# Kernel tuning notes

Hardware: AMD Instinct MI355X
Metric: run time of the kernel (lower is better)

Reference implementation:

```python
import jax, jax.numpy as jnp
import numpy as np

INPUT_SIZE = 4
HIDDEN = 2048
OUTPUT_SIZE = 2
NOISE_STD = 0.05
ALPHA = 0.2
RANK = 2
N_SUPPORTS = 2
GDIM = 2 * RANK + INPUT_SIZE  # gaussian_basis_dim default
BATCH = 32
SEQ = 1000


def setup_inputs() -> dict:
    key = jax.random.key(0)
    ks = jax.random.split(key, 8)
    inp = jax.random.normal(ks[0], (BATCH, SEQ, INPUT_SIZE), dtype=jnp.float32)
    noise = jax.random.normal(ks[1], (BATCH, SEQ, HIDDEN), dtype=jnp.float32)
    gaussian_basis = jax.random.normal(ks[2], (GDIM, HIDDEN), dtype=jnp.float32)
    # supports: block indicator masks over hidden units (equal split, weights=None)
    sup = np.zeros((N_SUPPORTS, HIDDEN), dtype=np.float32)
    l = HIDDEN // N_SUPPORTS
    for i in range(N_SUPPORTS):
        sup[i, l * i:l * (i + 1)] = 1.0
    supports = jnp.asarray(sup)
    wi_weights = jax.random.normal(ks[3], (INPUT_SIZE, N_SUPPORTS, GDIM), dtype=jnp.float32)
    m_weights = jax.random.normal(ks[4], (RANK, N_SUPPORTS, GDIM), dtype=jnp.float32) / jnp.sqrt(jnp.float32(HIDDEN))
    n_weights = jax.random.normal(ks[5], (RANK, N_SUPPORTS, GDIM), dtype=jnp.float32) / jnp.sqrt(jnp.float32(HIDDEN))
    wo_weights = jax.random.normal(ks[6], (OUTPUT_SIZE, N_SUPPORTS, GDIM), dtype=jnp.float32) / jnp.float32(HIDDEN)
    wi_biases = jnp.zeros((INPUT_SIZE, N_SUPPORTS), dtype=jnp.float32)
    m_biases = jnp.zeros((RANK, N_SUPPORTS), dtype=jnp.float32)
    n_biases = jnp.zeros((RANK, N_SUPPORTS), dtype=jnp.float32)
    h0_weights = jnp.zeros((N_SUPPORTS, GDIM), dtype=jnp.float32)
    return {
        "input": inp, "noise": noise,
        "wi_weights": wi_weights, "m_weights": m_weights, "n_weights": n_weights,
        "wo_weights": wo_weights, "wi_biases": wi_biases, "m_biases": m_biases,
        "n_biases": n_biases, "h0_weights": h0_weights,
        "gaussian_basis": gaussian_basis, "supports": supports,
    }


def _proxy_params(wi_weights, m_weights, n_weights, wo_weights,
                  wi_biases, m_biases, n_biases, h0_weights,
                  gaussian_basis, supports):
    # (X, S, G) @ (G, H) -> (X, S, H); mask by supports (S, H); sum over S
    def mix(w):
        return jnp.einsum('xsg,gh->xsh', w, gaussian_basis)
    wi = jnp.sum(mix(wi_weights) * supports, axis=1) + wi_biases @ supports      # (I, H)
    m = (jnp.sum(mix(m_weights) * supports, axis=1) + m_biases @ supports).T     # (H, R)
    n = (jnp.sum(mix(n_weights) * supports, axis=1) + n_biases @ supports).T     # (H, R)
    wo = jnp.sum(mix(wo_weights) * supports, axis=1).T                            # (H, O)
    h0 = jnp.sum((h0_weights @ gaussian_basis) * supports, axis=0)                # (H,)
    return wi, m, n, wo, h0


def reference(input, noise, wi_weights, m_weights, n_weights, wo_weights,
              wi_biases, m_biases, n_biases, h0_weights, gaussian_basis, supports):
    wi, m, n, wo, h0 = _proxy_params(wi_weights, m_weights, n_weights, wo_weights,
                                     wi_biases, m_biases, n_biases, h0_weights,
                                     gaussian_basis, supports)
    B = input.shape[0]
    # Precompute external input projection for all steps: (B, T, H)
    xin = jnp.einsum('bti,ih->bth', input, wi)
    h_init = jnp.broadcast_to(h0, (B, h0.shape[0]))
    r_init = jnp.tanh(h_init)

    noise_T = jnp.swapaxes(noise, 0, 1)  # (T, B, H)
    xin_T = jnp.swapaxes(xin, 0, 1)      # (T, B, H)

    def step(carry, xs):
        h, r = carry
        noise_t, xin_t = xs
        h = h + NOISE_STD * noise_t + ALPHA * (-h + (r @ n) @ m.T + xin_t)
        r = jnp.tanh(h)
        return (h, r), r

    _, rs = jax.lax.scan(step, (h_init, r_init), (noise_T, xin_T))  # rs: (T, B, H)
    output = jnp.einsum('tbh,ho->bto', rs, wo)  # (B, T, O)
    return output
```

## Files before the change

kernel.cpp:

```cpp
#include <hip/hip_runtime.h>

#define BATCH 32
#define SEQT 1000
#define INSZ 4
#define HID 2048
#define NOISE_STD 0.05f
#define ALPHA 0.2f
#define ONE_M_ALPHA (1.0f - ALPHA)

#define NTHREADS 256
#define NWAVES 4
#define EPT 8
#define NPAIR 4
#define PF 4

typedef float v2f __attribute__((ext_vector_type(2)));

__device__ __forceinline__ v2f pk_fma(v2f a, v2f b, v2f c) {
    v2f d; asm("v_pk_fma_f32 %0, %1, %2, %3" : "=v"(d) : "v"(a), "v"(b), "v"(c)); return d;
}
__device__ __forceinline__ v2f pk_mul(v2f a, v2f b) {
    v2f d; asm("v_pk_mul_f32 %0, %1, %2" : "=v"(d) : "v"(a), "v"(b)); return d;
}
__device__ __forceinline__ v2f pk_add(v2f a, v2f b) {
    v2f d; asm("v_pk_add_f32 %0, %1, %2" : "=v"(d) : "v"(a), "v"(b)); return d;
}
#define C2(v) (v2f{(v), (v)})

__device__ __forceinline__ void tree64_quad(float& a, float& b, float& c, float& d) {
    asm("s_nop 1\n\t"
        "v_add_f32_dpp %0, %0, %0 row_shr:1 row_mask:0xf bank_mask:0xf bound_ctrl:0\n\t"
        "v_add_f32_dpp %1, %1, %1 row_shr:1 row_mask:0xf bank_mask:0xf bound_ctrl:0\n\t"
        "v_add_f32_dpp %2, %2, %2 row_shr:1 row_mask:0xf bank_mask:0xf bound_ctrl:0\n\t"
        "v_add_f32_dpp %3, %3, %3 row_shr:1 row_mask:0xf bank_mask:0xf bound_ctrl:0\n\t"
        "v_add_f32_dpp %0, %0, %0 row_shr:2 row_mask:0xf bank_mask:0xf bound_ctrl:0\n\t"
        "v_add_f32_dpp %1, %1, %1 row_shr:2 row_mask:0xf bank_mask:0xf bound_ctrl:0\n\t"
        "v_add_f32_dpp %2, %2, %2 row_shr:2 row_mask:0xf bank_mask:0xf bound_ctrl:0\n\t"
        "v_add_f32_dpp %3, %3, %3 row_shr:2 row_mask:0xf bank_mask:0xf bound_ctrl:0\n\t"
        "v_add_f32_dpp %0, %0, %0 row_shr:4 row_mask:0xf bank_mask:0xf bound_ctrl:0\n\t"
        "v_add_f32_dpp %1, %1, %1 row_shr:4 row_mask:0xf bank_mask:0xf bound_ctrl:0\n\t"
        "v_add_f32_dpp %2, %2, %2 row_shr:4 row_mask:0xf bank_mask:0xf bound_ctrl:0\n\t"
        "v_add_f32_dpp %3, %3, %3 row_shr:4 row_mask:0xf bank_mask:0xf bound_ctrl:0\n\t"
        "v_add_f32_dpp %0, %0, %0 row_shr:8 row_mask:0xf bank_mask:0xf bound_ctrl:0\n\t"
        "v_add_f32_dpp %1, %1, %1 row_shr:8 row_mask:0xf bank_mask:0xf bound_ctrl:0\n\t"
        "v_add_f32_dpp %2, %2, %2 row_shr:8 row_mask:0xf bank_mask:0xf bound_ctrl:0\n\t"
        "v_add_f32_dpp %3, %3, %3 row_shr:8 row_mask:0xf bank_mask:0xf bound_ctrl:0\n\t"
        "v_add_f32_dpp %0, %0, %0 row_bcast:15 row_mask:0xf bank_mask:0xf bound_ctrl:0\n\t"
        "v_add_f32_dpp %1, %1, %1 row_bcast:15 row_mask:0xf bank_mask:0xf bound_ctrl:0\n\t"
        "v_add_f32_dpp %2, %2, %2 row_bcast:15 row_mask:0xf bank_mask:0xf bound_ctrl:0\n\t"
        "v_add_f32_dpp %3, %3, %3 row_bcast:15 row_mask:0xf bank_mask:0xf bound_ctrl:0\n\t"
        "v_add_f32_dpp %0, %0, %0 row_bcast:31 row_mask:0xf bank_mask:0xf bound_ctrl:0\n\t"
        "v_add_f32_dpp %1, %1, %1 row_bcast:31 row_mask:0xf bank_mask:0xf bound_ctrl:0\n\t"
        "v_add_f32_dpp %2, %2, %2 row_bcast:31 row_mask:0xf bank_mask:0xf bound_ctrl:0\n\t"
        "v_add_f32_dpp %3, %3, %3 row_bcast:31 row_mask:0xf bank_mask:0xf bound_ctrl:0"
        : "+v"(a), "+v"(b), "+v"(c), "+v"(d));
}

__device__ __forceinline__ void tree64_pair(float& a, float& b) {
    asm("s_nop 1\n\t"
        "v_add_f32_dpp %0, %0, %0 row_shr:1 row_mask:0xf bank_mask:0xf bound_ctrl:0\n\t"
        "v_add_f32_dpp %1, %1, %1 row_shr:1 row_mask:0xf bank_mask:0xf bound_ctrl:0\n\t"
        "v_add_f32_dpp %0, %0, %0 row_shr:2 row_mask:0xf bank_mask:0xf bound_ctrl:0\n\t"
        "v_add_f32_dpp %1, %1, %1 row_shr:2 row_mask:0xf bank_mask:0xf bound_ctrl:0\n\t"
        "v_add_f32_dpp %0, %0, %0 row_shr:4 row_mask:0xf bank_mask:0xf bound_ctrl:0\n\t"
        "v_add_f32_dpp %1, %1, %1 row_shr:4 row_mask:0xf bank_mask:0xf bound_ctrl:0\n\t"
        "v_add_f32_dpp %0, %0, %0 row_shr:8 row_mask:0xf bank_mask:0xf bound_ctrl:0\n\t"
        "v_add_f32_dpp %1, %1, %1 row_shr:8 row_mask:0xf bank_mask:0xf bound_ctrl:0\n\t"
        "v_add_f32_dpp %0, %0, %0 row_bcast:15 row_mask:0xf bank_mask:0xf bound_ctrl:0\n\t"
        "v_add_f32_dpp %1, %1, %1 row_bcast:15 row_mask:0xf bank_mask:0xf bound_ctrl:0\n\t"
        "v_add_f32_dpp %0, %0, %0 row_bcast:31 row_mask:0xf bank_mask:0xf bound_ctrl:0\n\t"
        "v_add_f32_dpp %1, %1, %1 row_bcast:31 row_mask:0xf bank_mask:0xf bound_ctrl:0"
        : "+v"(a), "+v"(b));
}

__device__ __forceinline__ void bfly4_quad(float& a, float& b, float& c, float& d) {
    asm("s_nop 1\n\t"
        "v_add_f32_dpp %0, %0, %0 quad_perm:[1,0,3,2] row_mask:0xf bank_mask:0xf\n\t"
        "v_add_f32_dpp %1, %1, %1 quad_perm:[1,0,3,2] row_mask:0xf bank_mask:0xf\n\t"
        "v_add_f32_dpp %2, %2, %2 quad_perm:[1,0,3,2] row_mask:0xf bank_mask:0xf\n\t"
        "v_add_f32_dpp %3, %3, %3 quad_perm:[1,0,3,2] row_mask:0xf bank_mask:0xf\n\t"
        "v_add_f32_dpp %0, %0, %0 quad_perm:[2,3,0,1] row_mask:0xf bank_mask:0xf\n\t"
        "v_add_f32_dpp %1, %1, %1 quad_perm:[2,3,0,1] row_mask:0xf bank_mask:0xf\n\t"
        "v_add_f32_dpp %2, %2, %2 quad_perm:[2,3,0,1] row_mask:0xf bank_mask:0xf\n\t"
        "v_add_f32_dpp %3, %3, %3 quad_perm:[2,3,0,1] row_mask:0xf bank_mask:0xf"
        : "+v"(a), "+v"(b), "+v"(c), "+v"(d));
}

__device__ __forceinline__ void bfly4_pair(float& a, float& b) {
    asm("s_nop 1\n\t"
        "v_add_f32_dpp %0, %0, %0 quad_perm:[1,0,3,2] row_mask:0xf bank_mask:0xf\n\t"
        "v_add_f32_dpp %1, %1, %1 quad_perm:[1,0,3,2] row_mask:0xf bank_mask:0xf\n\t"
        "v_add_f32_dpp %0, %0, %0 quad_perm:[2,3,0,1] row_mask:0xf bank_mask:0xf\n\t"
        "v_add_f32_dpp %1, %1, %1 quad_perm:[2,3,0,1] row_mask:0xf bank_mask:0xf"
        : "+v"(a), "+v"(b));
}

__device__ __forceinline__ v2f pade_tanh(v2f x) {
    const v2f x2  = pk_mul(x, x);
    const v2f num = pk_mul(x, pk_fma(x2, pk_add(x2, C2(105.0f)), C2(945.0f)));
    const v2f den = pk_fma(x2, pk_fma(x2, C2(15.0f), C2(420.0f)), C2(945.0f));
    v2f r;
    r.x = num.x * __builtin_amdgcn_rcpf(den.x);
    r.y = num.y * __builtin_amdgcn_rcpf(den.y);
    r.x = fminf(fmaxf(r.x, -1.0f), 1.0f);
    r.y = fminf(fmaxf(r.y, -1.0f), 1.0f);
    return r;
}

__device__ __forceinline__ float pade_tanh_s(float x) {
    const float x2 = x * x;
    const float num = x * fmaf(x2, x2 + 105.0f, 945.0f);
    const float den = fmaf(x2, fmaf(x2, 15.0f, 420.0f), 945.0f);
    float r = num * __builtin_amdgcn_rcpf(den);
    return fminf(fmaxf(r, -1.0f), 1.0f);
}

#define LDS_BARRIER() __asm__ volatile("s_waitcnt lgkmcnt(0)\ns_barrier" ::: "memory")

__global__ __launch_bounds__(NTHREADS)
void rnn_kernel(const float* __restrict__ input,
                const float* __restrict__ noise,
                const float* __restrict__ wi_w,
                const float* __restrict__ m_w,
                const float* __restrict__ n_w,
                const float* __restrict__ wo_w,
                const float* __restrict__ wi_b,
                const float* __restrict__ m_b,
                const float* __restrict__ n_b,
                const float* __restrict__ h0_w,
                const float* __restrict__ gb,
                const float* __restrict__ sup,
                float* __restrict__ out)
{
    __shared__ __align__(16) float2 sDup[SEQT][4];
    __shared__ __align__(16) float4 sW4[2][NWAVES][65];

    const int b    = blockIdx.x;
    const int tid  = threadIdx.x;
    const int wave = tid >> 6;
    const int lane = tid & 63;

    const float4* inRow4 = reinterpret_cast<const float4*>(input + (size_t)b * SEQT * INSZ);
    for (int i = tid; i < SEQT; i += NTHREADS) {
        const float4 v = inRow4[i];
        sDup[i][0] = make_float2(v.x, v.x);
        sDup[i][1] = make_float2(v.y, v.y);
        sDup[i][2] = make_float2(v.z, v.z);
        sDup[i][3] = make_float2(v.w, v.w);
    }

    v2f wiA[INSZ][NPAIR];
    v2f mA0v[NPAIR], mA1v[NPAIR], n0v[NPAIR], n1v[NPAIR], wo0v[NPAIR], wo1v[NPAIR], hv[NPAIR];
    v2f q0 = {0.f, 0.f}, q1 = q0, q2 = q0, q3 = q0;

    #pragma unroll
    for (int e = 0; e < EPT; ++e) {
        const int h = tid * EPT + e;
        const int pi = e >> 1, pc = e & 1;
        float gv[8];
        #pragma unroll
        for (int g = 0; g < 8; ++g) gv[g] = gb[g * HID + h];
        const float s0 = sup[h];
        const float s1 = sup[HID + h];

        auto mix = [&](const float* w) -> float {
            float a0 = 0.f, a1 = 0.f;
            #pragma unroll
            for (int g = 0; g < 8; ++g) { a0 += w[g] * gv[g]; a1 += w[8 + g] * gv[g]; }
            return s0 * a0 + s1 * a1;
        };

        #pragma unroll
        for (int i = 0; i < INSZ; ++i)
            wiA[i][pi][pc] = ALPHA * (mix(wi_w + i * 16) + wi_b[i * 2 + 0] * s0 + wi_b[i * 2 + 1] * s1);
        mA0v[pi][pc] = ALPHA * (mix(m_w)      + m_b[0] * s0 + m_b[1] * s1);
        mA1v[pi][pc] = ALPHA * (mix(m_w + 16) + m_b[2] * s0 + m_b[3] * s1);
        const float n0 = mix(n_w)      + n_b[0] * s0 + n_b[1] * s1;
        const float n1 = mix(n_w + 16) + n_b[2] * s0 + n_b[3] * s1;
        const float w0 = mix(wo_w);
        const float w1 = mix(wo_w + 16);
        n0v[pi][pc] = n0;  n1v[pi][pc] = n1;
        wo0v[pi][pc] = w0; wo1v[pi][pc] = w1;
        {
            float a0 = 0.f, a1 = 0.f;
            #pragma unroll
            for (int g = 0; g < 8; ++g) { a0 += h0_w[g] * gv[g]; a1 += h0_w[8 + g] * gv[g]; }
            const float h0v = s0 * a0 + s1 * a1;
            hv[pi][pc] = h0v;
            const float r = pade_tanh_s(h0v);
            q0[pc] += r * n0;  q1[pc] += r * n1;
            q2[pc] += r * w0;  q3[pc] += r * w1;
        }
    }

    const float4* nP4 = reinterpret_cast<const float4*>(noise + (size_t)b * SEQT * HID);
    const int rowStride = HID / 4;
    const int nbase = tid * 2;
    float4 na0 = nP4[0 * rowStride + nbase], nb0 = nP4[0 * rowStride + nbase + 1];
    float4 na1 = nP4[1 * rowStride + nbase], nb1 = nP4[1 * rowStride + nbase + 1];
    float4 na2 = nP4[2 * rowStride + nbase], nb2 = nP4[2 * rowStride + nbase + 1];
    float4 na3 = nP4[3 * rowStride + nbase], nb3 = nP4[3 * rowStride + nbase + 1];

    float* outRow = out + (size_t)b * SEQT * 2;

    __syncthreads();
    const float4* dRow = reinterpret_cast<const float4*>(sDup);
    float4 ivA0 = dRow[0], ivB0 = dRow[1];
    float4 ivA1 = dRow[2], ivB1 = dRow[3];
    float4 ivA2 = dRow[4], ivB2 = dRow[5];
    float4 ivA3 = dRow[6], ivB3 = dRow[7];

    const v2f cNS  = C2(NOISE_STD);
    const v2f cOMA = C2(ONE_M_ALPHA);

    auto do_step = [&](int t, int PAR, float4& nA, float4& nB, float4& ivAreg, float4& ivBreg) {
        float w0 = q0.x + q0.y;
        float w1 = q1.x + q1.y;
        float oz = q2.x + q2.y;
        float ow = q3.x + q3.y;
        tree64_quad(w0, w1, oz, ow);
        sW4[PAR][wave][lane] = make_float4(w0, w1, oz, ow);

        LDS_BARRIER();

        const float4 pr = sW4[PAR][lane & 3][63];

        const int tpre = (t + PF < SEQT) ? (t + PF) : (SEQT - 1);
        const float4 nv4a = nA, nv4b = nB;
        nA = nP4[(size_t)tpre * rowStride + nbase];
        nB = nP4[(size_t)tpre * rowStride + nbase + 1];
        const float4 ivA = ivAreg, ivB = ivBreg;
        ivAreg = dRow[2 * tpre];
        ivBreg = dRow[2 * tpre + 1];

        const v2f ix = {ivA.x, ivA.y}, iy = {ivA.z, ivA.w};
        const v2f iz = {ivB.x, ivB.y}, iw = {ivB.z, ivB.w};
        const v2f nn[NPAIR] = { {nv4a.x, nv4a.y}, {nv4a.z, nv4a.w},
                                {nv4b.x, nv4b.y}, {nv4b.z, nv4b.w} };
        v2f acc[NPAIR];
        #pragma unroll
        for (int p = 0; p < NPAIR; ++p) {
            acc[p] = pk_mul(wiA[0][p], ix);
            acc[p] = pk_fma(wiA[1][p], iy, acc[p]);
            acc[p] = pk_fma(wiA[2][p], iz, acc[p]);
            acc[p] = pk_fma(wiA[3][p], iw, acc[p]);
            acc[p] = pk_fma(nn[p], cNS, acc[p]);
            acc[p] = pk_fma(hv[p], cOMA, acc[p]);
        }

        float y0 = pr.x, y1 = pr.y, o0 = pr.z, o1 = pr.w;
        bfly4_quad(y0, y1, o0, o1);

        if (t >= 1 && tid == ((t & 3) << 6))
            *reinterpret_cast<float2*>(outRow + (t - 1) * 2) = make_float2(o0, o1);

        const v2f y0p = {y0, y0}, y1p = {y1, y1};
        v2f r[NPAIR];
        #pragma unroll
        for (int p = 0; p < NPAIR; ++p) {
            v2f h2 = pk_fma(mA1v[p], y1p, acc[p]);
            h2 = pk_fma(mA0v[p], y0p, h2);
            hv[p] = h2;
            r[p] = pade_tanh(h2);
        }
        q0 = pk_mul(r[0], n0v[0]);  q1 = pk_mul(r[0], n1v[0]);
        q2 = pk_mul(r[0], wo0v[0]); q3 = pk_mul(r[0], wo1v[0]);
        #pragma unroll
        for (int p = 1; p < NPAIR; ++p) {
            q0 = pk_fma(r[p], n0v[p],  q0);
            q1 = pk_fma(r[p], n1v[p],  q1);
            q2 = pk_fma(r[p], wo0v[p], q2);
            q3 = pk_fma(r[p], wo1v[p], q3);
        }
    };

    for (int t = 0; t < SEQT; t += PF) {
        do_step(t,     0, na0, nb0, ivA0, ivB0);
        do_step(t + 1, 1, na1, nb1, ivA1, ivB1);
        do_step(t + 2, 0, na2, nb2, ivA2, ivB2);
        do_step(t + 3, 1, na3, nb3, ivA3, ivB3);
    }

    {
        float a9 = q2.x + q2.y;
        float b9 = q3.x + q3.y;
        tree64_pair(a9, b9);
        sW4[0][wave][lane] = make_float4(a9, b9, 0.f, 0.f);
        LDS_BARRIER();
        const float4 pr = sW4[0][lane & 3][63];
        float x9 = pr.x, y9 = pr.y;
        bfly4_pair(x9, y9);
        if (tid == 0)
            *reinterpret_cast<float2*>(outRow + 999 * 2) = make_float2(x9, y9);
    }
}

extern "C" void kernel_launch(void* const* d_in, const int* in_sizes, int n_in,
                              void* d_out, int out_size, void* d_ws, size_t ws_size,
                              hipStream_t stream) {
    const float* input = (const float*)d_in[0];
    const float* noise = (const float*)d_in[1];
    const float* wi_w  = (const float*)d_in[2];
    const float* m_w   = (const float*)d_in[3];
    const float* n_w   = (const float*)d_in[4];
    const float* wo_w  = (const float*)d_in[5];
    const float* wi_b  = (const float*)d_in[6];
    const float* m_b   = (const float*)d_in[7];
    const float* n_b   = (const float*)d_in[8];
    const float* h0_w  = (const float*)d_in[9];
    const float* gb    = (const float*)d_in[10];
    const float* sup   = (const float*)d_in[11];
    float* out = (float*)d_out;

    rnn_kernel<<<dim3(BATCH), dim3(NTHREADS), 0, stream>>>(
        input, noise, wi_w, m_w, n_w, wo_w, wi_b, m_b, n_b, h0_w, gb, sup, out);
}
```

Measured before the change: 800.7 us.

## Pack two batch sequences per block and move barrier after independent FMAs

Each 512-thread block now runs two independent batch sequences in separate halves, each with its own LDS slices, and the grid shrinks to 16 blocks. The per-step LDS barrier is moved after the input/noise/h accumulation so that independent arithmetic can overlap barrier latency. The shared s_barrier now synchronizes both sequences together, coupling their step timing, and only half as many CUs are used.

```diff
diff --git a/kernel.cpp b/kernel.cpp
--- a/kernel.cpp
+++ b/kernel.cpp
@@ -8,7 +8,8 @@
 #define ALPHA 0.2f
 #define ONE_M_ALPHA (1.0f - ALPHA)
 
-#define NTHREADS 256
+#define NTHREADS 512
+#define NSEQ 2
 #define NWAVES 4
 #define EPT 8
 #define NPAIR 4
@@ -132,21 +133,26 @@
                 const float* __restrict__ sup,
                 float* __restrict__ out)
 {
-    __shared__ __align__(16) float2 sDup[SEQT][4];
-    __shared__ __align__(16) float4 sW4[2][NWAVES][65];
-
-    const int b    = blockIdx.x;
+    __shared__ __align__(16) float2 sDup[NSEQ][SEQT][4];
+    __shared__ __align__(16) float4 sW4[NSEQ][2][NWAVES][65];
+
     const int tid  = threadIdx.x;
-    const int wave = tid >> 6;
+    const int half = tid >> 8;
+    const int tl   = tid & 255;
+    const int wave = tl >> 6;
     const int lane = tid & 63;
-
-    const float4* inRow4 = reinterpret_cast<const float4*>(input + (size_t)b * SEQT * INSZ);
-    for (int i = tid; i < SEQT; i += NTHREADS) {
+    const int bb   = blockIdx.x * NSEQ + half;
+
+    float2 (*dup)[4] = sDup[half];
+    float4 (*sWh)[NWAVES][65] = sW4[half];
+
+    const float4* inRow4 = reinterpret_cast<const float4*>(input + (size_t)bb * SEQT * INSZ);
+    for (int i = tl; i < SEQT; i += 256) {
         const float4 v = inRow4[i];
-        sDup[i][0] = make_float2(v.x, v.x);
-        sDup[i][1] = make_float2(v.y, v.y);
-        sDup[i][2] = make_float2(v.z, v.z);
-        sDup[i][3] = make_float2(v.w, v.w);
+        dup[i][0] = make_float2(v.x, v.x);
+        dup[i][1] = make_float2(v.y, v.y);
+        dup[i][2] = make_float2(v.z, v.z);
+        dup[i][3] = make_float2(v.w, v.w);
     }
 
     v2f wiA[INSZ][NPAIR];
@@ -155,7 +161,7 @@
 
     #pragma unroll
     for (int e = 0; e < EPT; ++e) {
-        const int h = tid * EPT + e;
+        const int h = tl * EPT + e;
         const int pi = e >> 1, pc = e & 1;
         float gv[8];
         #pragma unroll
@@ -193,18 +199,18 @@
         }
     }
 
-    const float4* nP4 = reinterpret_cast<const float4*>(noise + (size_t)b * SEQT * HID);
+    const float4* nP4 = reinterpret_cast<const float4*>(noise + (size_t)bb * SEQT * HID);
     const int rowStride = HID / 4;
-    const int nbase = tid * 2;
+    const int nbase = tl * 2;
     float4 na0 = nP4[0 * rowStride + nbase], nb0 = nP4[0 * rowStride + nbase + 1];
     float4 na1 = nP4[1 * rowStride + nbase], nb1 = nP4[1 * rowStride + nbase + 1];
     float4 na2 = nP4[2 * rowStride + nbase], nb2 = nP4[2 * rowStride + nbase + 1];
     float4 na3 = nP4[3 * rowStride + nbase], nb3 = nP4[3 * rowStride + nbase + 1];
 
-    float* outRow = out + (size_t)b * SEQT * 2;
+    float* outRow = out + (size_t)bb * SEQT * 2;
 
     __syncthreads();
-    const float4* dRow = reinterpret_cast<const float4*>(sDup);
+    const float4* dRow = reinterpret_cast<const float4*>(dup);
     float4 ivA0 = dRow[0], ivB0 = dRow[1];
     float4 ivA1 = dRow[2], ivB1 = dRow[3];
     float4 ivA2 = dRow[4], ivB2 = dRow[5];
@@ -219,20 +225,10 @@
         float oz = q2.x + q2.y;
         float ow = q3.x + q3.y;
         tree64_quad(w0, w1, oz, ow);
-        sW4[PAR][wave][lane] = make_float4(w0, w1, oz, ow);
-
-        LDS_BARRIER();
-
-        const float4 pr = sW4[PAR][lane & 3][63];
-
-        const int tpre = (t + PF < SEQT) ? (t + PF) : (SEQT - 1);
+        sWh[PAR][wave][lane] = make_float4(w0, w1, oz, ow);
+
         const float4 nv4a = nA, nv4b = nB;
-        nA = nP4[(size_t)tpre * rowStride + nbase];
-        nB = nP4[(size_t)tpre * rowStride + nbase + 1];
         const float4 ivA = ivAreg, ivB = ivBreg;
-        ivAreg = dRow[2 * tpre];
-        ivBreg = dRow[2 * tpre + 1];
-
         const v2f ix = {ivA.x, ivA.y}, iy = {ivA.z, ivA.w};
         const v2f iz = {ivB.x, ivB.y}, iw = {ivB.z, ivB.w};
         const v2f nn[NPAIR] = { {nv4a.x, nv4a.y}, {nv4a.z, nv4a.w},
@@ -248,10 +244,20 @@
             acc[p] = pk_fma(hv[p], cOMA, acc[p]);
         }
 
+        LDS_BARRIER();
+
+        const float4 pr = sWh[PAR][lane & 3][63];
+
+        const int tpre = (t + PF < SEQT) ? (t + PF) : (SEQT - 1);
+        nA = nP4[(size_t)tpre * rowStride + nbase];
+        nB = nP4[(size_t)tpre * rowStride + nbase + 1];
+        ivAreg = dRow[2 * tpre];
+        ivBreg = dRow[2 * tpre + 1];
+
         float y0 = pr.x, y1 = pr.y, o0 = pr.z, o1 = pr.w;
         bfly4_quad(y0, y1, o0, o1);
 
-        if (t >= 1 && tid == ((t & 3) << 6))
+        if (t >= 1 && tl == ((t & 3) << 6))
             *reinterpret_cast<float2*>(outRow + (t - 1) * 2) = make_float2(o0, o1);
 
         const v2f y0p = {y0, y0}, y1p = {y1, y1};
@@ -285,12 +291,12 @@
         float a9 = q2.x + q2.y;
         float b9 = q3.x + q3.y;
         tree64_pair(a9, b9);
-        sW4[0][wave][lane] = make_float4(a9, b9, 0.f, 0.f);
+        sWh[0][wave][lane] = make_float4(a9, b9, 0.f, 0.f);
         LDS_BARRIER();
-        const float4 pr = sW4[0][lane & 3][63];
+        const float4 pr = sWh[0][lane & 3][63];
         float x9 = pr.x, y9 = pr.y;
         bfly4_pair(x9, y9);
-        if (tid == 0)
+        if (tl == 0)
             *reinterpret_cast<float2*>(outRow + 999 * 2) = make_float2(x9, y9);
     }
 }
@@ -312,6 +318,6 @@
     const float* sup   = (const float*)d_in[11];
     float* out = (float*)d_out;
 
-    rnn_kernel<<<dim3(BATCH), dim3(NTHREADS), 0, stream>>>(
+    rnn_kernel<<<dim3(BATCH / NSEQ), dim3(NTHREADS), 0, stream>>>(
         input, noise, wi_w, m_w, n_w, wo_w, wi_b, m_b, n_b, h0_w, gb, sup, out);
 }
```

New measurement: 997.7 us. 24.6% more time.

## Run each batch row on a single wavefront to remove per-step LDS barriers

Applied to the files above, without the earlier changes.

Shrinks the block from four waves to one 64-lane wave, with each lane owning 32 hidden units. The per-step cross-wave reduction through LDS plus s_barrier is replaced by a DPP tree and a readlane from lane 63. Input values are now read directly from global memory with a 2-step register prefetch instead of being staged in LDS. In exchange, each lane does four times more ALU work per step and holds many more registers, and noise prefetch depth drops from four steps to two.

```diff
diff --git a/kernel.cpp b/kernel.cpp
--- a/kernel.cpp
+++ b/kernel.cpp
@@ -8,11 +8,9 @@
 #define ALPHA 0.2f
 #define ONE_M_ALPHA (1.0f - ALPHA)
 
-#define NTHREADS 256
-#define NWAVES 4
-#define EPT 8
-#define NPAIR 4
-#define PF 4
+#define NTHREADS 64
+#define NPAIR 16
+#define NLD 8
 
 typedef float v2f __attribute__((ext_vector_type(2)));
 
@@ -73,28 +71,6 @@
         : "+v"(a), "+v"(b));
 }
 
-__device__ __forceinline__ void bfly4_quad(float& a, float& b, float& c, float& d) {
-    asm("s_nop 1\n\t"
-        "v_add_f32_dpp %0, %0, %0 quad_perm:[1,0,3,2] row_mask:0xf bank_mask:0xf\n\t"
-        "v_add_f32_dpp %1, %1, %1 quad_perm:[1,0,3,2] row_mask:0xf bank_mask:0xf\n\t"
-        "v_add_f32_dpp %2, %2, %2 quad_perm:[1,0,3,2] row_mask:0xf bank_mask:0xf\n\t"
-        "v_add_f32_dpp %3, %3, %3 quad_perm:[1,0,3,2] row_mask:0xf bank_mask:0xf\n\t"
-        "v_add_f32_dpp %0, %0, %0 quad_perm:[2,3,0,1] row_mask:0xf bank_mask:0xf\n\t"
-        "v_add_f32_dpp %1, %1, %1 quad_perm:[2,3,0,1] row_mask:0xf bank_mask:0xf\n\t"
-        "v_add_f32_dpp %2, %2, %2 quad_perm:[2,3,0,1] row_mask:0xf bank_mask:0xf\n\t"
-        "v_add_f32_dpp %3, %3, %3 quad_perm:[2,3,0,1] row_mask:0xf bank_mask:0xf"
-        : "+v"(a), "+v"(b), "+v"(c), "+v"(d));
-}
-
-__device__ __forceinline__ void bfly4_pair(float& a, float& b) {
-    asm("s_nop 1\n\t"
-        "v_add_f32_dpp %0, %0, %0 quad_perm:[1,0,3,2] row_mask:0xf bank_mask:0xf\n\t"
-        "v_add_f32_dpp %1, %1, %1 quad_perm:[1,0,3,2] row_mask:0xf bank_mask:0xf\n\t"
-        "v_add_f32_dpp %0, %0, %0 quad_perm:[2,3,0,1] row_mask:0xf bank_mask:0xf\n\t"
-        "v_add_f32_dpp %1, %1, %1 quad_perm:[2,3,0,1] row_mask:0xf bank_mask:0xf"
-        : "+v"(a), "+v"(b));
-}
-
 __device__ __forceinline__ v2f pade_tanh(v2f x) {
     const v2f x2  = pk_mul(x, x);
     const v2f num = pk_mul(x, pk_fma(x2, pk_add(x2, C2(105.0f)), C2(945.0f)));
@@ -115,9 +91,11 @@
     return fminf(fmaxf(r, -1.0f), 1.0f);
 }
 
-#define LDS_BARRIER() __asm__ volatile("s_waitcnt lgkmcnt(0)\ns_barrier" ::: "memory")
-
-__global__ __launch_bounds__(NTHREADS)
+__device__ __forceinline__ float readlane63(float x) {
+    return __int_as_float(__builtin_amdgcn_readlane(__float_as_int(x), 63));
+}
+
+__global__ __launch_bounds__(NTHREADS, 1)
 void rnn_kernel(const float* __restrict__ input,
                 const float* __restrict__ noise,
                 const float* __restrict__ wi_w,
@@ -132,127 +110,113 @@
                 const float* __restrict__ sup,
                 float* __restrict__ out)
 {
-    __shared__ __align__(16) float2 sDup[SEQT][4];
-    __shared__ __align__(16) float4 sW4[2][NWAVES][65];
-
     const int b    = blockIdx.x;
-    const int tid  = threadIdx.x;
-    const int wave = tid >> 6;
-    const int lane = tid & 63;
-
-    const float4* inRow4 = reinterpret_cast<const float4*>(input + (size_t)b * SEQT * INSZ);
-    for (int i = tid; i < SEQT; i += NTHREADS) {
-        const float4 v = inRow4[i];
-        sDup[i][0] = make_float2(v.x, v.x);
-        sDup[i][1] = make_float2(v.y, v.y);
-        sDup[i][2] = make_float2(v.z, v.z);
-        sDup[i][3] = make_float2(v.w, v.w);
-    }
+    const int lane = threadIdx.x;
 
     v2f wiA[INSZ][NPAIR];
     v2f mA0v[NPAIR], mA1v[NPAIR], n0v[NPAIR], n1v[NPAIR], wo0v[NPAIR], wo1v[NPAIR], hv[NPAIR];
     v2f q0 = {0.f, 0.f}, q1 = q0, q2 = q0, q3 = q0;
 
     #pragma unroll
-    for (int e = 0; e < EPT; ++e) {
-        const int h = tid * EPT + e;
-        const int pi = e >> 1, pc = e & 1;
-        float gv[8];
-        #pragma unroll
-        for (int g = 0; g < 8; ++g) gv[g] = gb[g * HID + h];
-        const float s0 = sup[h];
-        const float s1 = sup[HID + h];
-
-        auto mix = [&](const float* w) -> float {
-            float a0 = 0.f, a1 = 0.f;
+    for (int k = 0; k < NLD; ++k) {
+        #pragma unroll
+        for (int e = 0; e < 4; ++e) {
+            const int h = k * 256 + lane * 4 + e;
+            const int pi = 2 * k + (e >> 1), pc = e & 1;
+            float gv[8];
             #pragma unroll
-            for (int g = 0; g < 8; ++g) { a0 += w[g] * gv[g]; a1 += w[8 + g] * gv[g]; }
-            return s0 * a0 + s1 * a1;
-        };
-
-        #pragma unroll
-        for (int i = 0; i < INSZ; ++i)
-            wiA[i][pi][pc] = ALPHA * (mix(wi_w + i * 16) + wi_b[i * 2 + 0] * s0 + wi_b[i * 2 + 1] * s1);
-        mA0v[pi][pc] = ALPHA * (mix(m_w)      + m_b[0] * s0 + m_b[1] * s1);
-        mA1v[pi][pc] = ALPHA * (mix(m_w + 16) + m_b[2] * s0 + m_b[3] * s1);
-        const float n0 = mix(n_w)      + n_b[0] * s0 + n_b[1] * s1;
-        const float n1 = mix(n_w + 16) + n_b[2] * s0 + n_b[3] * s1;
-        const float w0 = mix(wo_w);
-        const float w1 = mix(wo_w + 16);
-        n0v[pi][pc] = n0;  n1v[pi][pc] = n1;
-        wo0v[pi][pc] = w0; wo1v[pi][pc] = w1;
-        {
-            float a0 = 0.f, a1 = 0.f;
+            for (int g = 0; g < 8; ++g) gv[g] = gb[g * HID + h];
+            const float s0 = sup[h];
+            const float s1 = sup[HID + h];
+
+            auto mix = [&](const float* w) -> float {
+                float a0 = 0.f, a1 = 0.f;
+                #pragma unroll
+                for (int g = 0; g < 8; ++g) { a0 += w[g] * gv[g]; a1 += w[8 + g] * gv[g]; }
+                return s0 * a0 + s1 * a1;
+            };
+
             #pragma unroll
-            for (int g = 0; g < 8; ++g) { a0 += h0_w[g] * gv[g]; a1 += h0_w[8 + g] * gv[g]; }
-            const float h0v = s0 * a0 + s1 * a1;
-            hv[pi][pc] = h0v;
-            const float r = pade_tanh_s(h0v);
-            q0[pc] += r * n0;  q1[pc] += r * n1;
-            q2[pc] += r * w0;  q3[pc] += r * w1;
+            for (int i = 0; i < INSZ; ++i)
+                wiA[i][pi][pc] = ALPHA * (mix(wi_w + i * 16) + wi_b[i * 2 + 0] * s0 + wi_b[i * 2 + 1] * s1);
+            mA0v[pi][pc] = ALPHA * (mix(m_w)      + m_b[0] * s0 + m_b[1] * s1);
+            mA1v[pi][pc] = ALPHA * (mix(m_w + 16) + m_b[2] * s0 + m_b[3] * s1);
+            const float n0 = mix(n_w)      + n_b[0] * s0 + n_b[1] * s1;
+            const float n1 = mix(n_w + 16) + n_b[2] * s0 + n_b[3] * s1;
+            const float w0 = mix(wo_w);
+            const float w1 = mix(wo_w + 16);
+            n0v[pi][pc] = n0;  n1v[pi][pc] = n1;
+            wo0v[pi][pc] = w0; wo1v[pi][pc] = w1;
+            {
+                float a0 = 0.f, a1 = 0.f;
+                #pragma unroll
+                for (int g = 0; g < 8; ++g) { a0 += h0_w[g] * gv[g]; a1 += h0_w[8 + g] * gv[g]; }
+                const float h0v = s0 * a0 + s1 * a1;
+                hv[pi][pc] = h0v;
+                const float r = pade_tanh_s(h0v);
+                q0[pc] += r * n0;  q1[pc] += r * n1;
+                q2[pc] += r * w0;  q3[pc] += r * w1;
+            }
         }
     }
 
-    const float4* nP4 = reinterpret_cast<const float4*>(noise + (size_t)b * SEQT * HID);
-    const int rowStride = HID / 4;
-    const int nbase = tid * 2;
-    float4 na0 = nP4[0 * rowStride + nbase], nb0 = nP4[0 * rowStride + nbase + 1];
-    float4 na1 = nP4[1 * rowStride + nbase], nb1 = nP4[1 * rowStride + nbase + 1];
-    float4 na2 = nP4[2 * rowStride + nbase], nb2 = nP4[2 * rowStride + nbase + 1];
-    float4 na3 = nP4[3 * rowStride + nbase], nb3 = nP4[3 * rowStride + nbase + 1];
+    const float4* nP4 = reinterpret_cast<const float4*>(noise + (size_t)b * SEQT * HID) + lane;
+    float4 nbA[NLD], nbB[NLD];
+    #pragma unroll
+    for (int k = 0; k < NLD; ++k) nbA[k] = nP4[(size_t)0 * 512 + k * 64];
+    #pragma unroll
+    for (int k = 0; k < NLD; ++k) nbB[k] = nP4[(size_t)1 * 512 + k * 64];
+
+    const float4* inRow4 = reinterpret_cast<const float4*>(input + (size_t)b * SEQT * INSZ);
+    float4 inA = inRow4[0];
+    float4 inB = inRow4[1];
 
     float* outRow = out + (size_t)b * SEQT * 2;
-
-    __syncthreads();
-    const float4* dRow = reinterpret_cast<const float4*>(sDup);
-    float4 ivA0 = dRow[0], ivB0 = dRow[1];
-    float4 ivA1 = dRow[2], ivB1 = dRow[3];
-    float4 ivA2 = dRow[4], ivB2 = dRow[5];
-    float4 ivA3 = dRow[6], ivB3 = dRow[7];
 
     const v2f cNS  = C2(NOISE_STD);
     const v2f cOMA = C2(ONE_M_ALPHA);
 
-    auto do_step = [&](int t, int PAR, float4& nA, float4& nB, float4& ivAreg, float4& ivBreg) {
+    auto do_step = [&](int t, float4* nb, float4& invReg) {
         float w0 = q0.x + q0.y;
         float w1 = q1.x + q1.y;
         float oz = q2.x + q2.y;
         float ow = q3.x + q3.y;
         tree64_quad(w0, w1, oz, ow);
-        sW4[PAR][wave][lane] = make_float4(w0, w1, oz, ow);
-
-        LDS_BARRIER();
-
-        const float4 pr = sW4[PAR][lane & 3][63];
-
-        const int tpre = (t + PF < SEQT) ? (t + PF) : (SEQT - 1);
-        const float4 nv4a = nA, nv4b = nB;
-        nA = nP4[(size_t)tpre * rowStride + nbase];
-        nB = nP4[(size_t)tpre * rowStride + nbase + 1];
-        const float4 ivA = ivAreg, ivB = ivBreg;
-        ivAreg = dRow[2 * tpre];
-        ivBreg = dRow[2 * tpre + 1];
-
-        const v2f ix = {ivA.x, ivA.y}, iy = {ivA.z, ivA.w};
-        const v2f iz = {ivB.x, ivB.y}, iw = {ivB.z, ivB.w};
-        const v2f nn[NPAIR] = { {nv4a.x, nv4a.y}, {nv4a.z, nv4a.w},
-                                {nv4b.x, nv4b.y}, {nv4b.z, nv4b.w} };
+
+        const float y0 = readlane63(w0);
+        const float y1 = readlane63(w1);
+
+        if (t >= 1 && lane == 63)
+            *reinterpret_cast<float2*>(outRow + (t - 1) * 2) = make_float2(oz, ow);
+
+        const float4 inv = invReg;
+        const v2f bx = {inv.x, inv.x}, by = {inv.y, inv.y};
+        const v2f bz = {inv.z, inv.z}, bw = {inv.w, inv.w};
         v2f acc[NPAIR];
         #pragma unroll
-        for (int p = 0; p < NPAIR; ++p) {
-            acc[p] = pk_mul(wiA[0][p], ix);
-            acc[p] = pk_fma(wiA[1][p], iy, acc[p]);
-            acc[p] = pk_fma(wiA[2][p], iz, acc[p]);
-            acc[p] = pk_fma(wiA[3][p], iw, acc[p]);
-            acc[p] = pk_fma(nn[p], cNS, acc[p]);
-            acc[p] = pk_fma(hv[p], cOMA, acc[p]);
-        }
-
-        float y0 = pr.x, y1 = pr.y, o0 = pr.z, o1 = pr.w;
-        bfly4_quad(y0, y1, o0, o1);
-
-        if (t >= 1 && tid == ((t & 3) << 6))
-            *reinterpret_cast<float2*>(outRow + (t - 1) * 2) = make_float2(o0, o1);
+        for (int k = 0; k < NLD; ++k) {
+            const float4 nv = nb[k];
+            const v2f nlo = {nv.x, nv.y}, nhi = {nv.z, nv.w};
+            v2f a0 = pk_mul(wiA[0][2 * k], bx);
+            v2f a1 = pk_mul(wiA[0][2 * k + 1], bx);
+            a0 = pk_fma(wiA[1][2 * k],     by, a0);
+            a1 = pk_fma(wiA[1][2 * k + 1], by, a1);
+            a0 = pk_fma(wiA[2][2 * k],     bz, a0);
+            a1 = pk_fma(wiA[2][2 * k + 1], bz, a1);
+            a0 = pk_fma(wiA[3][2 * k],     bw, a0);
+            a1 = pk_fma(wiA[3][2 * k + 1], bw, a1);
+            a0 = pk_fma(nlo, cNS, a0);
+            a1 = pk_fma(nhi, cNS, a1);
+            a0 = pk_fma(hv[2 * k],     cOMA, a0);
+            a1 = pk_fma(hv[2 * k + 1], cOMA, a1);
+            acc[2 * k] = a0;
+            acc[2 * k + 1] = a1;
+        }
+
+        const int tpre = (t + 2 < SEQT) ? (t + 2) : (SEQT - 1);
+        #pragma unroll
+        for (int k = 0; k < NLD; ++k) nb[k] = nP4[(size_t)tpre * 512 + k * 64];
+        invReg = inRow4[tpre];
 
         const v2f y0p = {y0, y0}, y1p = {y1, y1};
         v2f r[NPAIR];
@@ -274,24 +238,17 @@
         }
     };
 
-    for (int t = 0; t < SEQT; t += PF) {
-        do_step(t,     0, na0, nb0, ivA0, ivB0);
-        do_step(t + 1, 1, na1, nb1, ivA1, ivB1);
-        do_step(t + 2, 0, na2, nb2, ivA2, ivB2);
-        do_step(t + 3, 1, na3, nb3, ivA3, ivB3);
+    for (int t = 0; t < SEQT; t += 2) {
+        do_step(t,     nbA, inA);
+        do_step(t + 1, nbB, inB);
     }
 
     {
         float a9 = q2.x + q2.y;
         float b9 = q3.x + q3.y;
         tree64_pair(a9, b9);
-        sW4[0][wave][lane] = make_float4(a9, b9, 0.f, 0.f);
-        LDS_BARRIER();
-        const float4 pr = sW4[0][lane & 3][63];
-        float x9 = pr.x, y9 = pr.y;
-        bfly4_pair(x9, y9);
-        if (tid == 0)
-            *reinterpret_cast<float2*>(outRow + 999 * 2) = make_float2(x9, y9);
+        if (lane == 63)
+            *reinterpret_cast<float2*>(outRow + 999 * 2) = make_float2(a9, b9);
     }
 }
 
```

New measurement: 1.939 ms. +142.2%, slower.
